# Performance work log

Measured on AMD Instinct MI355X. Metric: run time of the kernel, lower is better.

## Reference

```python
import jax, jax.numpy as jnp
from jax import lax
import numpy as np

N, E = 10000, 120000
IN_DIM = 128
HID = 32        # hidden_dim
HEADS = 8
OUT = 32        # out_dim
HD = HID * HEADS  # 256
EPS = 1e-5


def _bn(x, g, b):
    # BatchNorm1d (training-mode batch stats, deterministic reference)
    mu = x.mean(0)
    var = x.var(0)
    return g * (x - mu) * lax.rsqrt(var + EPS) + b


def _seg_softmax(logits, seg, n):
    # softmax over edges grouped by destination node, per head
    m = jax.ops.segment_max(logits, seg, num_segments=n)
    ex = jnp.exp(logits - m[seg])
    s = jax.ops.segment_sum(ex, seg, num_segments=n)
    return ex / (s[seg] + 1e-16)


def _gat_layer(h, src, dst, fc_w, a_l, a_r, bn_g, bn_b, heads, out, residual):
    n = h.shape[0]
    h_in = h
    feat = (h @ fc_w).reshape(n, heads, out)      # [N,H,D]
    el = (feat * a_l).sum(-1)                     # [N,H]
    er = (feat * a_r).sum(-1)
    logits = jax.nn.leaky_relu(el[src] + er[dst], 0.2)  # [E,H]
    alpha = _seg_softmax(logits, dst, n)
    rst = jax.ops.segment_sum(alpha[..., None] * feat[src], dst, num_segments=n)
    rst = rst.reshape(n, heads * out)
    rst = _bn(rst, bn_g, bn_b)
    rst = jax.nn.elu(rst)
    if residual:
        rst = h_in + rst
    return rst


def setup_inputs():
    key = jax.random.key(0)
    ks = jax.random.split(key, 20)
    s = 0.02
    d = {}
    d["h"] = jax.random.normal(ks[0], (N, IN_DIM), jnp.float32)
    d["e"] = jax.random.normal(ks[1], (E, IN_DIM), jnp.float32)
    d["src"] = jax.random.randint(ks[2], (E,), 0, N, jnp.int32)
    d["dst"] = jax.random.randint(ks[3], (E,), 0, N, jnp.int32)
    d["W_emb"] = jax.random.normal(ks[4], (IN_DIM, HD)) * s
    d["b_emb"] = jnp.zeros((HD,))
    d["W_p1"] = jax.random.normal(ks[5], (IN_DIM, HID * HID)) * s
    d["b_p1"] = jnp.zeros((HID * HID,))
    d["W_p2"] = jax.random.normal(ks[6], (IN_DIM, HID)) * s
    d["b_p2"] = jnp.zeros((HID,))
    d["W_conv"] = jax.random.normal(ks[7], (1, 2, 3)) * s  # Conv1d(2->1,k=3)
    d["b_conv"] = jnp.zeros((1,))
    d["W_ep2"] = jax.random.normal(ks[8], (IN_DIM, HD)) * s
    d["b_ep2"] = jnp.zeros((HD,))
    d["W_ep3"] = jax.random.normal(ks[9], (HID, HD)) * s
    d["b_ep3"] = jnp.zeros((HD,))
    d["bn_g"] = jnp.ones((HD,))
    d["bn_b"] = jnp.zeros((HD,))
    d["fc1"] = jax.random.normal(ks[10], (HD, HD)) * s
    d["al1"] = jax.random.normal(ks[11], (HEADS, HID)) * s
    d["ar1"] = jax.random.normal(ks[12], (HEADS, HID)) * s
    d["g1"] = jnp.ones((HD,))
    d["b1"] = jnp.zeros((HD,))
    d["fc2"] = jax.random.normal(ks[13], (HD, OUT)) * s
    d["al2"] = jax.random.normal(ks[14], (1, OUT)) * s
    d["ar2"] = jax.random.normal(ks[15], (1, OUT)) * s
    d["g2"] = jnp.ones((OUT,))
    d["b2"] = jnp.zeros((OUT,))
    return d


def reference(h, e, src, dst, W_emb, b_emb, W_p1, b_p1, W_p2, b_p2,
              W_conv, b_conv, W_ep2, b_ep2, W_ep3, b_ep3, bn_g, bn_b,
              fc1, al1, ar1, g1, b1, fc2, al2, ar2, g2, b2):
    # local edge feature: Conv1d over stacked (src,dst) node feats
    edge = jnp.stack([h[src], h[dst]], axis=1)  # [E,2,IN_DIM]
    conv = lax.conv_general_dilated(edge, W_conv, (1,), [(1, 1)],
                                    dimension_numbers=("NCH", "OIH", "NCH"))
    lr_local = conv[:, 0, :] + b_conv[0]         # [E,IN_DIM]
    lr_e_local = lr_local @ W_ep2 + b_ep2        # [E,HD]
    # low-rank global affinity: mm[i,j,k] = sum_d p1[i,k,d]*p2[j,d],
    # gathered only at edges (same math as the dense NxNxHID tensor)
    p1 = (h @ W_p1 + b_p1).reshape(-1, HID, HID)  # [N,HID,HID]
    p2 = h @ W_p2 + b_p2                          # [N,HID]
    lr_glob = jnp.einsum("ekd,ed->ek", p1[src], p2[dst])  # [E,HID]
    lr_e_global = lr_glob @ W_ep3 + b_ep3        # [E,HD]
    e_feat = jax.nn.relu(_bn(lr_e_local + lr_e_global, bn_g, bn_b))
    del e_feat  # default 'dgl' GATLayer ignores e; kept for faithfulness of math
    hh = h @ W_emb + b_emb                       # embedding_h
    hh = _gat_layer(hh, src, dst, fc1, al1, ar1, g1, b1, HEADS, HID, True)
    hh = _gat_layer(hh, src, dst, fc2, al2, ar2, g2, b2, 1, OUT, False)
    return hh
```

## Files before the change

### kernel.cpp

```cpp
#include <hip/hip_runtime.h>
#include <hip/hip_bf16.h>
#include <math.h>


#define HDIM 256
#define NHEADS 8
#define ODIM 32

typedef unsigned short u16;
typedef __attribute__((ext_vector_type(8))) short short8;
typedef __attribute__((ext_vector_type(4))) float f32x4;

__device__ __forceinline__ float bf2f(u16 u) { return __uint_as_float(((unsigned)u) << 16); }
__device__ __forceinline__ u16 f2bf(float f) {
    unsigned x = __float_as_uint(f);
    return (u16)((x + 0x7FFFu + ((x >> 16) & 1u)) >> 16);
}

__global__ __launch_bounds__(256) void prep_kernel(const float* __restrict__ in_h, const float* __restrict__ W_emb,
                                                   const float* __restrict__ fc1, const float* __restrict__ fc2,
                                                   const int* __restrict__ dstv, int* __restrict__ deg,
                                                   u16* __restrict__ Ah, u16* __restrict__ Bemb,
                                                   u16* __restrict__ Bfc1, u16* __restrict__ Bfc2,
                                                   int n4, int E, int N) {
    int job = blockIdx.y;
    int idx = blockIdx.x * 256 + threadIdx.x;
    if (job == 0) {
        if (idx >= n4) return;
        float4 v = ((const float4*)in_h)[idx];
        ushort4 o = {f2bf(v.x), f2bf(v.y), f2bf(v.z), f2bf(v.w)};
        ((ushort4*)Ah)[idx] = o;
        return;
    }
    if (job == 4) {
        if (idx < E) {
            unsigned d = (unsigned)dstv[idx];
            if (d < (unsigned)N) atomicAdd(&deg[d], 1);
        }
        return;
    }
    const float* B;
    u16* O;
    int K, NC;
    if (job == 1) { B = W_emb; O = Bemb; K = 128; NC = 256; }
    else if (job == 2) { B = fc1; O = Bfc1; K = 256; NC = 256; }
    else { B = fc2; O = Bfc2; K = 256; NC = 32; }
    int KB = K / 32;
    int TOT = (NC / 16) * KB * 64;
    if (idx >= TOT) return;
    int lane = idx & 63;
    int kb = (idx >> 6) % KB;
    int ct = (idx >> 6) / KB;
    int n = ct * 16 + (lane & 15);
    int k0 = kb * 32 + (lane >> 4) * 8;
    u16* dst = O + (size_t)idx * 8;
#pragma unroll
    for (int j = 0; j < 8; j++) dst[j] = f2bf(B[(size_t)(k0 + j) * NC + n]);
}

__global__ __launch_bounds__(256) void scan_kernel(const int* __restrict__ deg, int* __restrict__ offs,
                                                   int* __restrict__ cursor, int n) {
    __shared__ int wsum[4];
    int t = threadIdx.x;
    int chunk = (n + 255) / 256;
    int lo = t * chunk, hi = lo + chunk;
    if (hi > n) hi = n;
    if (lo > n) lo = n;
    int s = 0;
    for (int i = lo; i < hi; i++) s += deg[i];
    int v = s;
#pragma unroll
    for (int d = 1; d < 64; d <<= 1) {
        int nb = __shfl_up(v, d, 64);
        if ((t & 63) >= d) v += nb;
    }
    if ((t & 63) == 63) wsum[t >> 6] = v;
    __syncthreads();
    int woff = 0;
#pragma unroll
    for (int w = 0; w < 4; w++)
        if (w < (t >> 6)) woff += wsum[w];
    int run = woff + v - s;
    for (int i = lo; i < hi; i++) {
        offs[i] = run;
        cursor[i] = run;
        run += deg[i];
    }
    if (t == 255) offs[n] = run;
}

__global__ __launch_bounds__(256) void fused_emb_fc1(const u16* __restrict__ Ah, const u16* __restrict__ Bemb,
                                                     const float* __restrict__ bemb, const u16* __restrict__ Bfc1,
                                                     const float* __restrict__ al, const float* __restrict__ ar,
                                                     u16* __restrict__ hh, u16* __restrict__ feat1,
                                                     u16* __restrict__ el, u16* __restrict__ er,
                                                     const int* __restrict__ src, const int* __restrict__ dstv,
                                                     int* __restrict__ cursor, int* __restrict__ srcs,
                                                     int M, int NB, int E, int N) {
    if ((int)blockIdx.x >= NB) {
        int i = ((int)blockIdx.x - NB) * 256 + (int)threadIdx.x;
        if (i < E) {
            unsigned d = (unsigned)dstv[i];
            if (d < (unsigned)N) {
                int p = atomicAdd(&cursor[d], 1);
                if ((unsigned)p < (unsigned)E) srcs[p] = src[i];
            }
        }
        return;
    }
    __shared__ u16 tile[64 * 256];
    const int t = threadIdx.x;
    const int lane = t & 63, wq = t >> 6;
    const int rb = (int)blockIdx.x * 64;
    const int m = lane & 15, q = lane >> 4;
    const int row = rb + wq * 16 + m;

    short8 a0[4];
#pragma unroll
    for (int kb = 0; kb < 4; kb++) {
        if (row < M) a0[kb] = *(const short8*)(Ah + (size_t)row * 128 + kb * 32 + q * 8);
        else a0[kb] = (short8){0, 0, 0, 0, 0, 0, 0, 0};
    }
    const short8* B8 = (const short8*)Bemb;
#pragma unroll 1
    for (int ct = 0; ct < 16; ct++) {
        f32x4 acc = {0.f, 0.f, 0.f, 0.f};
#pragma unroll
        for (int kb = 0; kb < 4; kb++)
            acc = __builtin_amdgcn_mfma_f32_16x16x32_bf16(a0[kb], B8[(ct * 4 + kb) * 64 + lane], acc, 0, 0, 0);
        float bv = bemb[ct * 16 + m];
#pragma unroll
        for (int r = 0; r < 4; r++) {
            int rl = wq * 16 + q * 4 + r;
            int ro = rb + rl;
            u16 hv = 0;
            if (ro < M) {
                hv = f2bf(acc[r] + bv);
                hh[(size_t)ro * 256 + ct * 16 + m] = hv;
            }
            int byte = rl * 512 + (ct * 16 + m) * 2;
            tile[(byte ^ ((rl & 7) << 4)) >> 1] = hv;
        }
    }
    __syncthreads();

    short8 af[8];
    {
        int rl = wq * 16 + m;
#pragma unroll
        for (int kb = 0; kb < 8; kb++) {
            int byte = rl * 512 + kb * 64 + q * 16;
            af[kb] = *(const short8*)(tile + ((byte ^ ((rl & 7) << 4)) >> 1));
        }
    }
    __syncthreads();

    const short8* Bf = (const short8*)Bfc1;
#pragma unroll 1
    for (int ct = 0; ct < 16; ct++) {
        f32x4 acc = {0.f, 0.f, 0.f, 0.f};
#pragma unroll
        for (int kb = 0; kb < 8; kb++)
            acc = __builtin_amdgcn_mfma_f32_16x16x32_bf16(af[kb], Bf[(ct * 8 + kb) * 64 + lane], acc, 0, 0, 0);
#pragma unroll
        for (int r = 0; r < 4; r++) {
            int rl = wq * 16 + q * 4 + r;
            int ro = rb + rl;
            u16 v = 0;
            if (ro < M) {
                v = f2bf(acc[r]);
                feat1[(size_t)ro * 256 + ct * 16 + m] = v;
            }
            tile[rl * 256 + ct * 16 + m] = v;
        }
    }
    __syncthreads();

#pragma unroll
    for (int task = t; task < 512; task += 256) {
        int nl = task >> 3, h2 = task & 7;
        int node = rb + nl;
        if (node >= M) continue;
        float a_ = 0.f, b_ = 0.f;
#pragma unroll
        for (int d = 0; d < 32; d++) {
            float fv = bf2f(tile[nl * 256 + h2 * 32 + d]);
            a_ += fv * al[h2 * 32 + d];
            b_ += fv * ar[h2 * 32 + d];
        }
        el[node * 8 + h2] = f2bf(a_);
        er[node * 8 + h2] = f2bf(b_);
    }
}

__device__ __forceinline__ float edgew(float l) {
    l = (l > 0.f) ? l : 0.2f * l;
    l = fminf(fmaxf(l, -30.f), 30.f);
    return __expf(l);
}

__global__ __launch_bounds__(256) void agg1_fused(const u16* __restrict__ feat, const u16* __restrict__ el,
                                                  const u16* __restrict__ er, const int* __restrict__ offs,
                                                  const int* __restrict__ srcs, u16* __restrict__ rst, int N, int E) {
    const int node = blockIdx.x * 4 + (threadIdx.x >> 6);
    const int lane = threadIdx.x & 63;
    if (node >= N) return;
    const int h = lane >> 3;
    int beg = offs[node], end = offs[node + 1];
    if (beg < 0) beg = 0;
    if (end > E) end = E;
    float ern = bf2f(er[node * 8 + h]);
    float ax = 0.f, ay = 0.f, az = 0.f, aw = 0.f, sw = 0.f;
    int j = beg;
    int end4 = beg + ((end - beg) & ~3);
    for (; j < end4; j += 4) {
        int s0 = srcs[j], s1 = srcs[j + 1], s2 = srcs[j + 2], s3 = srcs[j + 3];
        unsigned c0 = (unsigned)s0 < (unsigned)N, c1 = (unsigned)s1 < (unsigned)N;
        unsigned c2 = (unsigned)s2 < (unsigned)N, c3 = (unsigned)s3 < (unsigned)N;
        s0 = c0 ? s0 : 0; s1 = c1 ? s1 : 0; s2 = c2 ? s2 : 0; s3 = c3 ? s3 : 0;
        u16 e0 = el[s0 * 8 + h], e1 = el[s1 * 8 + h], e2 = el[s2 * 8 + h], e3 = el[s3 * 8 + h];
        ushort4 f0 = *(const ushort4*)(feat + (size_t)s0 * 256 + lane * 4);
        ushort4 f1 = *(const ushort4*)(feat + (size_t)s1 * 256 + lane * 4);
        ushort4 f2 = *(const ushort4*)(feat + (size_t)s2 * 256 + lane * 4);
        ushort4 f3 = *(const ushort4*)(feat + (size_t)s3 * 256 + lane * 4);
        float w0 = c0 ? edgew(bf2f(e0) + ern) : 0.f;
        float w1 = c1 ? edgew(bf2f(e1) + ern) : 0.f;
        float w2 = c2 ? edgew(bf2f(e2) + ern) : 0.f;
        float w3 = c3 ? edgew(bf2f(e3) + ern) : 0.f;
        sw += w0 + w1 + w2 + w3;
        ax += w0 * bf2f(f0.x) + w1 * bf2f(f1.x) + w2 * bf2f(f2.x) + w3 * bf2f(f3.x);
        ay += w0 * bf2f(f0.y) + w1 * bf2f(f1.y) + w2 * bf2f(f2.y) + w3 * bf2f(f3.y);
        az += w0 * bf2f(f0.z) + w1 * bf2f(f1.z) + w2 * bf2f(f2.z) + w3 * bf2f(f3.z);
        aw += w0 * bf2f(f0.w) + w1 * bf2f(f1.w) + w2 * bf2f(f2.w) + w3 * bf2f(f3.w);
    }
    for (; j < end; j++) {
        int s = srcs[j];
        if ((unsigned)s >= (unsigned)N) continue;
        float wv = edgew(bf2f(el[s * 8 + h]) + ern);
        ushort4 f4 = *(const ushort4*)(feat + (size_t)s * 256 + lane * 4);
        sw += wv;
        ax += wv * bf2f(f4.x);
        ay += wv * bf2f(f4.y);
        az += wv * bf2f(f4.z);
        aw += wv * bf2f(f4.w);
    }
    float inv = 1.f / (sw + 1e-16f);
    ushort4 o;
    o.x = f2bf(ax * inv); o.y = f2bf(ay * inv); o.z = f2bf(az * inv); o.w = f2bf(aw * inv);
    *(ushort4*)(rst + (size_t)node * 256 + lane * 4) = o;
}

__global__ __launch_bounds__(256) void bn_stats256(const u16* __restrict__ X, float* __restrict__ stats,
                                                   int rows, int RPB) {
    int t = threadIdx.x;
    int rbeg = blockIdx.x * RPB;
    int rend = rbeg + RPB;
    if (rend > rows) rend = rows;
    float s = 0.f, s2 = 0.f;
    for (int r = rbeg; r < rend; r++) {
        float x = bf2f(X[(long)r * 256 + t]);
        s += x;
        s2 += x * x;
    }
    atomicAdd(&stats[t], s);
    atomicAdd(&stats[256 + t], s2);
}

__global__ __launch_bounds__(256) void bn_stats32(const float* __restrict__ X, float* __restrict__ stats,
                                                  int rows, int RPB) {
    __shared__ float ss[256], ss2[256];
    int t = threadIdx.x, c = t & 31, rs = t >> 5;
    int rbeg = blockIdx.x * RPB;
    int rend = rbeg + RPB;
    if (rend > rows) rend = rows;
    float s = 0.f, s2 = 0.f;
    for (int r = rbeg + rs; r < rend; r += 8) {
        float x = X[(long)r * 32 + c];
        s += x;
        s2 += x * x;
    }
    ss[t] = s;
    ss2[t] = s2;
    __syncthreads();
    if (t < 32) {
        for (int j = 32; j < 256; j += 32) { s += ss[t + j]; s2 += ss2[t + j]; }
        atomicAdd(&stats[c], s);
        atomicAdd(&stats[32 + c], s2);
    }
}

__global__ __launch_bounds__(256) void gemm_fc2_fused(const u16* __restrict__ rst, const u16* __restrict__ hh,
                                                      const float* __restrict__ stats, const float* __restrict__ g,
                                                      const float* __restrict__ b, const u16* __restrict__ Bsw,
                                                      const float* __restrict__ al2, const float* __restrict__ ar2,
                                                      float* __restrict__ feat2, float* __restrict__ el2,
                                                      float* __restrict__ er2, int M, float invN) {
    __shared__ float sc[256], sh[256];
    __shared__ float tile[64][32];
    const int t = threadIdx.x;
    {
        float mu = stats[t] * invN;
        float var = fmaxf(stats[256 + t] * invN - mu * mu, 0.f);
        float s = g[t] * rsqrtf(var + 1e-5f);
        sc[t] = s;
        sh[t] = b[t] - mu * s;
    }
    __syncthreads();
    const int lane = t & 63, wq = t >> 6;
    const int rb = blockIdx.x * 64;
    const int m = lane & 15, q = lane >> 4;
    const int row = rb + wq * 16 + m;
    short8 a[8];
#pragma unroll
    for (int kb = 0; kb < 8; kb++) {
        if (row < M) {
            int k0 = kb * 32 + q * 8;
            ushort4 r01 = *(const ushort4*)(rst + (size_t)row * 256 + k0);
            ushort4 r23 = *(const ushort4*)(rst + (size_t)row * 256 + k0 + 4);
            ushort4 h01 = *(const ushort4*)(hh + (size_t)row * 256 + k0);
            ushort4 h23 = *(const ushort4*)(hh + (size_t)row * 256 + k0 + 4);
            u16 rv[8] = {r01.x, r01.y, r01.z, r01.w, r23.x, r23.y, r23.z, r23.w};
            u16 hv[8] = {h01.x, h01.y, h01.z, h01.w, h23.x, h23.y, h23.z, h23.w};
            short8 av;
#pragma unroll
            for (int j = 0; j < 8; j++) {
                int c = k0 + j;
                float y = sc[c] * bf2f(rv[j]) + sh[c];
                y = (y > 0.f) ? y : expm1f(y);
                av[j] = (short)f2bf(bf2f(hv[j]) + y);
            }
            a[kb] = av;
        } else a[kb] = (short8){0, 0, 0, 0, 0, 0, 0, 0};
    }
    const short8* B8 = (const short8*)Bsw;
#pragma unroll
    for (int ct = 0; ct < 2; ct++) {
        f32x4 acc = {0.f, 0.f, 0.f, 0.f};
#pragma unroll
        for (int kb = 0; kb < 8; kb++)
            acc = __builtin_amdgcn_mfma_f32_16x16x32_bf16(a[kb], B8[(ct * 8 + kb) * 64 + lane], acc, 0, 0, 0);
#pragma unroll
        for (int r = 0; r < 4; r++) {
            int rl = wq * 16 + q * 4 + r;
            int ro = rb + rl;
            float v = 0.f;
            if (ro < M) {
                v = acc[r];
                feat2[(size_t)ro * 32 + ct * 16 + m] = v;
            }
            tile[rl][ct * 16 + m] = v;
        }
    }
    __syncthreads();
    if (t < 64) {
        int node = rb + t;
        if (node < M) {
            float a_ = 0.f, b_ = 0.f;
#pragma unroll
            for (int d = 0; d < 32; d++) {
                float fv = tile[t][d];
                a_ += fv * al2[d];
                b_ += fv * ar2[d];
            }
            el2[node] = a_;
            er2[node] = b_;
        }
    }
}

__global__ __launch_bounds__(256) void agg2_fused(const float* __restrict__ feat, const float* __restrict__ el,
                                                  const float* __restrict__ er, const int* __restrict__ offs,
                                                  const int* __restrict__ srcs, float* __restrict__ rst,
                                                  int N, int E) {
    const int t = threadIdx.x;
    const int node = blockIdx.x * 8 + (t >> 5);
    const int d = t & 31;
    if (node >= N) return;
    int beg = offs[node], end = offs[node + 1];
    if (beg < 0) beg = 0;
    if (end > E) end = E;
    float ern = er[node];
    float acc = 0.f, sw = 0.f;
#pragma unroll 2
    for (int j = beg; j < end; j++) {
        int s = srcs[j];
        if ((unsigned)s >= (unsigned)N) continue;
        float wv = edgew(el[s] + ern);
        sw += wv;
        acc += wv * feat[(size_t)s * 32 + d];
    }
    rst[(size_t)node * 32 + d] = acc / (sw + 1e-16f);
}

__global__ __launch_bounds__(256) void bn_apply2(const float* __restrict__ rst, const float* __restrict__ stats,
                                                 const float* __restrict__ g, const float* __restrict__ b,
                                                 float* __restrict__ out, int total, float invN) {
    int idx = blockIdx.x * 256 + threadIdx.x;
    if (idx >= total) return;
    int c = idx & 31;
    float mu = stats[c] * invN;
    float var = fmaxf(stats[32 + c] * invN - mu * mu, 0.f);
    float y = g[c] * (rst[idx] - mu) * rsqrtf(var + 1e-5f) + b[c];
    y = (y > 0.f) ? y : expm1f(y);
    out[idx] = y;
}

extern "C" void kernel_launch(void* const* d_in, const int* in_sizes, int n_in, void* d_out, int out_size, void* d_ws,
                              size_t ws_size, hipStream_t stream) {
    const int N = out_size / ODIM;
    const int E = in_sizes[2];

    const int* src = (const int*)d_in[2];
    const int* dst = (const int*)d_in[3];
    const float* in_h = (const float*)d_in[0];
    const float* W_emb = (const float*)d_in[4];  const float* b_emb = (const float*)d_in[5];
    const float* fc1 = (const float*)d_in[18];   const float* al1 = (const float*)d_in[19];
    const float* ar1 = (const float*)d_in[20];
    const float* g1 = (const float*)d_in[21];    const float* b1 = (const float*)d_in[22];
    const float* fc2 = (const float*)d_in[23];   const float* al2 = (const float*)d_in[24];
    const float* ar2 = (const float*)d_in[25];
    const float* g2 = (const float*)d_in[26];    const float* b2 = (const float*)d_in[27];
    float* out = (float*)d_out;

    char* base = (char*)d_ws;
    size_t off = 0;
    auto alloc = [&](size_t bytes) { void* p = base + off; off += (bytes + 63) & ~63ull; return p; };
    char* zb   = (char*)alloc((size_t)N * 4 + 512 * 4 + 64 * 4);
    int* deg   = (int*)zb;
    float* stats  = (float*)(zb + (size_t)N * 4);
    float* stats2 = stats + 512;
    int* offs  = (int*)alloc((size_t)(N + 1) * 4);
    int* cursor = (int*)alloc((size_t)N * 4);
    int* srcs  = (int*)alloc((size_t)E * 4);
    u16* Ah    = (u16*)alloc((size_t)N * 128 * 2);
    u16* Bemb  = (u16*)alloc((size_t)128 * 256 * 2);
    u16* Bfc1  = (u16*)alloc((size_t)256 * 256 * 2);
    u16* Bfc2  = (u16*)alloc((size_t)256 * 32 * 2);
    u16* hh    = (u16*)alloc((size_t)N * HDIM * 2);
    u16* feat1 = (u16*)alloc((size_t)N * HDIM * 2);
    u16* el1   = (u16*)alloc((size_t)N * 8 * 2);
    u16* er1   = (u16*)alloc((size_t)N * 8 * 2);
    u16* rst   = (u16*)alloc((size_t)N * HDIM * 2);
    float* feat2 = (float*)alloc((size_t)N * 32 * 4);
    float* el2 = (float*)alloc((size_t)N * 4);
    float* er2 = (float*)alloc((size_t)N * 4);
    float* rst2 = (float*)alloc((size_t)N * 32 * 4);

    const int NB64 = (N + 63) / 64;
    const int NBF = (E + 255) / 256;

    hipMemsetAsync(zb, 0, (size_t)N * 4 + 512 * 4 + 64 * 4, stream);
    prep_kernel<<<dim3((N * 128 / 4 + 255) / 256, 5), 256, 0, stream>>>(in_h, W_emb, fc1, fc2, dst, deg,
                                                                        Ah, Bemb, Bfc1, Bfc2, N * 128 / 4, E, N);
    scan_kernel<<<1, 256, 0, stream>>>(deg, offs, cursor, N);
    fused_emb_fc1<<<NB64 + NBF, 256, 0, stream>>>(Ah, Bemb, b_emb, Bfc1, al1, ar1, hh, feat1, el1, er1,
                                                  src, dst, cursor, srcs, N, NB64, E, N);
    agg1_fused<<<(N + 3) / 4, 256, 0, stream>>>(feat1, el1, er1, offs, srcs, rst, N, E);
    bn_stats256<<<(N + 39) / 40, 256, 0, stream>>>(rst, stats, N, 40);
    gemm_fc2_fused<<<NB64, 256, 0, stream>>>(rst, hh, stats, g1, b1, Bfc2, al2, ar2, feat2, el2, er2, N, 1.f / N);
    agg2_fused<<<(N + 7) / 8, 256, 0, stream>>>(feat2, el2, er2, offs, srcs, rst2, N, E);
    bn_stats32<<<(N + 63) / 64, 256, 0, stream>>>(rst2, stats2, N, 64);
    bn_apply2<<<(N * ODIM + 255) / 256, 256, 0, stream>>>(rst2, stats2, g2, b2, out, N * ODIM, 1.f / N);
}
```

Measured before the change: 276.5 us.

## Split CSR fill into its own kernel and shrink GEMM row tiles to 16

The CSR fill blocks, which used to be appended to the fused embedding/fc1 GEMM launch, now run as a separate kernel. The GEMM kernel now processes 16 rows per block instead of 64. Each of the four waves handles a quarter of the output column tiles, and the LDS tile shrinks from 32 KB to 8 KB. This gives roughly four times as many blocks, for better occupancy and spread across CUs. The cost is an extra kernel launch, B matrices re-read by four times as many blocks, and only half the threads doing the el/er reduction.

```diff
diff --git a/kernel.cpp b/kernel.cpp
--- a/kernel.cpp
+++ b/kernel.cpp
@@ -89,41 +89,40 @@
     if (t == 255) offs[n] = run;
 }
 
+__global__ __launch_bounds__(256) void fill_kernel(const int* __restrict__ src, const int* __restrict__ dstv,
+                                                   int* __restrict__ cursor, int* __restrict__ srcs, int E, int N) {
+    int i = blockIdx.x * 256 + threadIdx.x;
+    if (i < E) {
+        unsigned d = (unsigned)dstv[i];
+        if (d < (unsigned)N) {
+            int p = atomicAdd(&cursor[d], 1);
+            if ((unsigned)p < (unsigned)E) srcs[p] = src[i];
+        }
+    }
+}
+
 __global__ __launch_bounds__(256) void fused_emb_fc1(const u16* __restrict__ Ah, const u16* __restrict__ Bemb,
                                                      const float* __restrict__ bemb, const u16* __restrict__ Bfc1,
                                                      const float* __restrict__ al, const float* __restrict__ ar,
                                                      u16* __restrict__ hh, u16* __restrict__ feat1,
-                                                     u16* __restrict__ el, u16* __restrict__ er,
-                                                     const int* __restrict__ src, const int* __restrict__ dstv,
-                                                     int* __restrict__ cursor, int* __restrict__ srcs,
-                                                     int M, int NB, int E, int N) {
-    if ((int)blockIdx.x >= NB) {
-        int i = ((int)blockIdx.x - NB) * 256 + (int)threadIdx.x;
-        if (i < E) {
-            unsigned d = (unsigned)dstv[i];
-            if (d < (unsigned)N) {
-                int p = atomicAdd(&cursor[d], 1);
-                if ((unsigned)p < (unsigned)E) srcs[p] = src[i];
-            }
-        }
-        return;
-    }
-    __shared__ u16 tile[64 * 256];
+                                                     u16* __restrict__ el, u16* __restrict__ er, int M) {
+    __shared__ u16 tile[16 * 256];
     const int t = threadIdx.x;
-    const int lane = t & 63, wq = t >> 6;
-    const int rb = (int)blockIdx.x * 64;
+    const int lane = t & 63, w = t >> 6;
+    const int rb = (int)blockIdx.x * 16;
     const int m = lane & 15, q = lane >> 4;
-    const int row = rb + wq * 16 + m;
+    const int arow = rb + m;
 
     short8 a0[4];
 #pragma unroll
     for (int kb = 0; kb < 4; kb++) {
-        if (row < M) a0[kb] = *(const short8*)(Ah + (size_t)row * 128 + kb * 32 + q * 8);
+        if (arow < M) a0[kb] = *(const short8*)(Ah + (size_t)arow * 128 + kb * 32 + q * 8);
         else a0[kb] = (short8){0, 0, 0, 0, 0, 0, 0, 0};
     }
     const short8* B8 = (const short8*)Bemb;
-#pragma unroll 1
-    for (int ct = 0; ct < 16; ct++) {
+#pragma unroll
+    for (int ct2 = 0; ct2 < 4; ct2++) {
+        const int ct = w * 4 + ct2;
         f32x4 acc = {0.f, 0.f, 0.f, 0.f};
 #pragma unroll
         for (int kb = 0; kb < 4; kb++)
@@ -131,7 +130,7 @@
         float bv = bemb[ct * 16 + m];
 #pragma unroll
         for (int r = 0; r < 4; r++) {
-            int rl = wq * 16 + q * 4 + r;
+            int rl = q * 4 + r;
             int ro = rb + rl;
             u16 hv = 0;
             if (ro < M) {
@@ -146,7 +145,7 @@
 
     short8 af[8];
     {
-        int rl = wq * 16 + m;
+        int rl = m;
 #pragma unroll
         for (int kb = 0; kb < 8; kb++) {
             int byte = rl * 512 + kb * 64 + q * 16;
@@ -156,15 +155,16 @@
     __syncthreads();
 
     const short8* Bf = (const short8*)Bfc1;
-#pragma unroll 1
-    for (int ct = 0; ct < 16; ct++) {
+#pragma unroll
+    for (int ct2 = 0; ct2 < 4; ct2++) {
+        const int ct = w * 4 + ct2;
         f32x4 acc = {0.f, 0.f, 0.f, 0.f};
 #pragma unroll
         for (int kb = 0; kb < 8; kb++)
             acc = __builtin_amdgcn_mfma_f32_16x16x32_bf16(af[kb], Bf[(ct * 8 + kb) * 64 + lane], acc, 0, 0, 0);
 #pragma unroll
         for (int r = 0; r < 4; r++) {
-            int rl = wq * 16 + q * 4 + r;
+            int rl = q * 4 + r;
             int ro = rb + rl;
             u16 v = 0;
             if (ro < M) {
@@ -176,20 +176,20 @@
     }
     __syncthreads();
 
-#pragma unroll
-    for (int task = t; task < 512; task += 256) {
-        int nl = task >> 3, h2 = task & 7;
+    if (t < 128) {
+        int nl = t >> 3, h2 = t & 7;
         int node = rb + nl;
-        if (node >= M) continue;
-        float a_ = 0.f, b_ = 0.f;
-#pragma unroll
-        for (int d = 0; d < 32; d++) {
-            float fv = bf2f(tile[nl * 256 + h2 * 32 + d]);
-            a_ += fv * al[h2 * 32 + d];
-            b_ += fv * ar[h2 * 32 + d];
-        }
-        el[node * 8 + h2] = f2bf(a_);
-        er[node * 8 + h2] = f2bf(b_);
+        if (node < M) {
+            float a_ = 0.f, b_ = 0.f;
+#pragma unroll
+            for (int d = 0; d < 32; d++) {
+                float fv = bf2f(tile[nl * 256 + h2 * 32 + d]);
+                a_ += fv * al[h2 * 32 + d];
+                b_ += fv * ar[h2 * 32 + d];
+            }
+            el[node * 8 + h2] = f2bf(a_);
+            er[node * 8 + h2] = f2bf(b_);
+        }
     }
 }
 
@@ -446,15 +446,15 @@
     float* er2 = (float*)alloc((size_t)N * 4);
     float* rst2 = (float*)alloc((size_t)N * 32 * 4);
 
+    const int NB16 = (N + 15) / 16;
     const int NB64 = (N + 63) / 64;
-    const int NBF = (E + 255) / 256;
 
     hipMemsetAsync(zb, 0, (size_t)N * 4 + 512 * 4 + 64 * 4, stream);
     prep_kernel<<<dim3((N * 128 / 4 + 255) / 256, 5), 256, 0, stream>>>(in_h, W_emb, fc1, fc2, dst, deg,
                                                                         Ah, Bemb, Bfc1, Bfc2, N * 128 / 4, E, N);
     scan_kernel<<<1, 256, 0, stream>>>(deg, offs, cursor, N);
-    fused_emb_fc1<<<NB64 + NBF, 256, 0, stream>>>(Ah, Bemb, b_emb, Bfc1, al1, ar1, hh, feat1, el1, er1,
-                                                  src, dst, cursor, srcs, N, NB64, E, N);
+    fill_kernel<<<(E + 255) / 256, 256, 0, stream>>>(src, dst, cursor, srcs, E, N);
+    fused_emb_fc1<<<NB16, 256, 0, stream>>>(Ah, Bemb, b_emb, Bfc1, al1, ar1, hh, feat1, el1, er1, N);
     agg1_fused<<<(N + 3) / 4, 256, 0, stream>>>(feat1, el1, er1, offs, srcs, rst, N, E);
     bn_stats256<<<(N + 39) / 40, 256, 0, stream>>>(rst, stats, N, 40);
     gemm_fc2_fused<<<NB64, 256, 0, stream>>>(rst, hh, stats, g1, b1, Bfc2, al2, ar2, feat2, el2, er2, N, 1.f / N);
```

After: 259.4 us. 6.2% less time.
